# Performance work log

Hardware: AMD Instinct MI355X
Metric: run time of the kernel (lower is better)

## Reference

```python
import jax, jax.numpy as jnp
import numpy as np

B, C, H, W = 2, 192, 64, 64
HEADS, KS = 6, 7
HD = C // HEADS


def setup_inputs() -> dict:
    key = jax.random.key(0)
    ks = jax.random.split(key, 6)
    s = 0.02
    return {
        "x": jax.random.normal(ks[0], (B, C, H, W), jnp.float32),
        "W_qkv1": jax.random.normal(ks[1], (3 * C, C, 1, 1), jnp.float32) * s,
        "b_qkv1": jnp.zeros((3 * C,), jnp.float32),
        "W_qkv2": jax.random.normal(ks[2], (3 * C, 1, 3, 3), jnp.float32) * s,  # depthwise
        "b_qkv2": jnp.zeros((3 * C,), jnp.float32),
        "temperature": jnp.ones((HEADS, 1, 1, 1), jnp.float32),
        "rpb": jax.random.normal(ks[3], (HEADS, 2 * KS - 1, 2 * KS - 1), jnp.float32) * s,
        "W_proj": jax.random.normal(ks[4], (C, C, 1, 1), jnp.float32) * s,
        "b_proj": jnp.zeros((C,), jnp.float32),
    }


def _conv(x, w, b, pad, groups=1):
    y = jax.lax.conv_general_dilated(
        x, w, (1, 1), pad,
        dimension_numbers=("NCHW", "OIHW", "NCHW"),
        feature_group_count=groups)
    return y + b[None, :, None, None]


def _l2norm(t, eps=1e-12):
    n = jnp.sqrt(jnp.sum(t * t, axis=-1, keepdims=True))
    return t / jnp.maximum(n, eps)


def _nbr_idx(L, K):
    # NATTEN shifted-window neighborhood (dilation=1): window start clamped to image.
    start = jnp.clip(jnp.arange(L) - K // 2, 0, L - K)
    idx = start[:, None] + jnp.arange(K)[None, :]        # [L,K] absolute neighbor index
    rel = idx - jnp.arange(L)[:, None] + (K - 1)         # [L,K] rpb table index
    return idx, rel


def _forward(x, W_qkv1, b_qkv1, W_qkv2, b_qkv2, temperature, rpb, W_proj, b_proj):
    Bq, Cq, Hh, Ww = x.shape
    heads = rpb.shape[0]
    K = (rpb.shape[1] + 1) // 2
    hd = Cq // heads
    qkv = _conv(_conv(x, W_qkv1, b_qkv1, "VALID"), W_qkv2, b_qkv2, "SAME", groups=3 * Cq)
    qkv = qkv.reshape(Bq, 3, heads, hd, Hh, Ww).transpose(1, 0, 2, 4, 5, 3)  # [3,B,h,H,W,d]
    q, k, v = qkv[0], qkv[1], qkv[2]
    q = _l2norm(q)
    k = _l2norm(k)
    idx_i, rel_i = _nbr_idx(Hh, K)
    idx_j, rel_j = _nbr_idx(Ww, K)
    ii = idx_i[:, None, :, None]  # [H,1,K,1]
    jj = idx_j[None, :, None, :]  # [1,W,1,K] -> broadcast [H,W,K,K]
    k_nb = k[:, :, ii, jj, :]     # [B,h,H,W,K,K,d]
    attn = jnp.einsum("bhijd,bhijkld->bhijkl", q, k_nb)
    bias = rpb[:, rel_i[:, None, :, None], rel_j[None, :, None, :]]  # [h,H,W,K,K]
    attn = (attn + bias[None]) * temperature.reshape(1, heads, 1, 1, 1, 1)
    attn = jax.nn.softmax(attn.reshape(Bq, heads, Hh, Ww, K * K), axis=-1)
    v_nb = v[:, :, ii, jj, :].reshape(Bq, heads, Hh, Ww, K * K, hd)
    out = jnp.einsum("bhijk,bhijkd->bhijd", attn, v_nb)
    out = out.transpose(0, 1, 4, 2, 3).reshape(Bq, Cq, Hh, Ww)
    return _conv(out, W_proj, b_proj, "VALID")


def reference(x, W_qkv1, b_qkv1, W_qkv2, b_qkv2, temperature, rpb, W_proj, b_proj):
    return _forward(x, W_qkv1, b_qkv1, W_qkv2, b_qkv2, temperature, rpb, W_proj, b_proj)
```

## Files before the change

### kernel.cpp

```cpp
#include <hip/hip_runtime.h>
#include <math.h>

#define HW 4096

typedef __attribute__((ext_vector_type(8))) short short8;
typedef __attribute__((ext_vector_type(8))) _Float16 half8;
typedef __attribute__((ext_vector_type(4))) float floatx4;

__device__ inline float bflo(unsigned u) { return __uint_as_float(u << 16); }
__device__ inline float bfhi(unsigned u) { return __uint_as_float(u & 0xffff0000u); }
__device__ inline unsigned short f2bf(float x) {
    unsigned u = __float_as_uint(x);
    return (unsigned short)((u + 0x7fffu + ((u >> 16) & 1u)) >> 16);
}
__device__ inline unsigned f2bf2(float lo, float hi) {
    unsigned a = __float_as_uint(lo), b = __float_as_uint(hi);
    a = (a + 0x7fffu + ((a >> 16) & 1u)) >> 16;
    b = (b + 0x7fffu + ((b >> 16) & 1u)) & 0xffff0000u;
    return a | b;
}
__device__ inline unsigned short f2h(float x) {
    _Float16 h = (_Float16)x;
    return __builtin_bit_cast(unsigned short, h);
}


__global__ __launch_bounds__(256) void k_gq(const float* __restrict__ x,
    const float* __restrict__ W1, const float* __restrict__ b1,
    unsigned short* __restrict__ qkv)
{
    __shared__ __align__(16) unsigned short As[64 * 200];
    __shared__ __align__(16) unsigned short Bs[64 * 200];
    const int t = threadIdx.x;
    const int m0 = blockIdx.x * 64;
    const int n0 = blockIdx.y * 64;
    const int w = t >> 6, lane = t & 63;
    const int b = m0 >> 12, px0 = m0 & 4095;
    {
        const float* xb = x + ((size_t)(b * 192) << 12) + px0 + lane;
        const int cb = w * 48;
        #pragma unroll
        for (int r4 = 0; r4 < 12; ++r4) {
            float v0 = xb[(size_t)(cb + r4 * 4 + 0) << 12];
            float v1 = xb[(size_t)(cb + r4 * 4 + 1) << 12];
            float v2 = xb[(size_t)(cb + r4 * 4 + 2) << 12];
            float v3 = xb[(size_t)(cb + r4 * 4 + 3) << 12];
            *(uint2*)&As[lane * 200 + cb + r4 * 4] =
                make_uint2(f2bf2(v0, v1), f2bf2(v2, v3));
        }
    }
    #pragma unroll
    for (int pass = 0; pass < 12; ++pass) {
        int idx = pass * 256 + t;
        int row = idx / 48, ch = idx - row * 48;
        float4 wv = *(const float4*)&W1[(size_t)(n0 + row) * 192 + ch * 4];
        *(uint2*)&Bs[row * 200 + ch * 4] =
            make_uint2(f2bf2(wv.x, wv.y), f2bf2(wv.z, wv.w));
    }
    __syncthreads();
    const int lm = lane & 15, lq = lane >> 4;
    floatx4 acc[4] = {};
    #pragma unroll
    for (int ks = 0; ks < 6; ++ks) {
        short8 bf = *(const short8*)&Bs[(w * 16 + lm) * 200 + ks * 32 + lq * 8];
        #pragma unroll
        for (int mt = 0; mt < 4; ++mt) {
            short8 af = *(const short8*)&As[(mt * 16 + lm) * 200 + ks * 32 + lq * 8];
            acc[mt] = __builtin_amdgcn_mfma_f32_16x16x32_bf16(af, bf, acc[mt], 0, 0, 0);
        }
    }
    __syncthreads();
    const float bias = b1[n0 + w * 16 + lm];
    #pragma unroll
    for (int mt = 0; mt < 4; ++mt)
        #pragma unroll
        for (int r = 0; r < 4; ++r)
            As[(mt * 16 + lq * 4 + r) * 72 + w * 16 + lm] = f2bf(acc[mt][r] + bias);
    __syncthreads();
    #pragma unroll
    for (int pass = 0; pass < 2; ++pass) {
        int idx = pass * 256 + t;
        int m = idx >> 3, n8 = idx & 7;
        uint4 val = *(const uint4*)&As[m * 72 + n8 * 8];
        int oc = n0 + n8 * 8;
        int g = oc >> 5, d = oc & 31;
        *(uint4*)&qkv[((((size_t)(b * 18 + g) << 12) + px0 + m) << 5) + d] = val;
    }
}

__global__ __launch_bounds__(256) void k_dw(const unsigned short* __restrict__ in,
    const float* __restrict__ W2, const float* __restrict__ b2,
    unsigned short* __restrict__ outq)
{
    __shared__ float wsm[288];
    __shared__ float bsm[32];
    const int t = threadIdx.x;
    const int bg = blockIdx.y;
    const int g = (bg >= 18) ? bg - 18 : bg;
    const int cbase = (g / 6) * 192 + (g % 6) * 32;
    for (int idx = t; idx < 288; idx += 256)
        wsm[idx] = W2[(cbase + (idx & 31)) * 9 + (idx >> 5)];
    if (t < 32) bsm[t] = b2[cbase + t];
    __syncthreads();
    const int px = (blockIdx.x << 6) + (t >> 2);
    const int d8 = t & 3;
    const int i = px >> 6, j = px & 63;
    const unsigned short* base = in + ((size_t)bg << 17);
    float acc[8];
    #pragma unroll
    for (int e = 0; e < 8; ++e) acc[e] = bsm[d8 * 8 + e];
    #pragma unroll
    for (int di = -1; di <= 1; ++di) {
        int ii = i + di;
        if (ii < 0 || ii > 63) continue;
        #pragma unroll
        for (int dj = -1; dj <= 1; ++dj) {
            int jj = j + dj;
            if (jj < 0 || jj > 63) continue;
            int tap = (di + 1) * 3 + dj + 1;
            uint4 u = *(const uint4*)(base + ((((ii << 6) + jj) << 5) + d8 * 8));
            const float* wt = &wsm[tap * 32 + d8 * 8];
            acc[0] = fmaf(bflo(u.x), wt[0], acc[0]);
            acc[1] = fmaf(bfhi(u.x), wt[1], acc[1]);
            acc[2] = fmaf(bflo(u.y), wt[2], acc[2]);
            acc[3] = fmaf(bfhi(u.y), wt[3], acc[3]);
            acc[4] = fmaf(bflo(u.z), wt[4], acc[4]);
            acc[5] = fmaf(bfhi(u.z), wt[5], acc[5]);
            acc[6] = fmaf(bflo(u.w), wt[6], acc[6]);
            acc[7] = fmaf(bfhi(u.w), wt[7], acc[7]);
        }
    }
    uint4 o;
    o.x = f2bf2(acc[0], acc[1]); o.y = f2bf2(acc[2], acc[3]);
    o.z = f2bf2(acc[4], acc[5]); o.w = f2bf2(acc[6], acc[7]);
    *(uint4*)(outq + ((size_t)bg << 17) + ((size_t)px << 5) + d8 * 8) = o;
}

__global__ __launch_bounds__(256) void k_attn(const unsigned short* __restrict__ qkv,
    const float* __restrict__ temp, const float* __restrict__ rpb,
    unsigned short* __restrict__ attnO)
{
    __shared__ __align__(16) char lds[45224];
    unsigned short* Ks  = (unsigned short*)lds;
    unsigned short* Ps  = (unsigned short*)lds;
    unsigned short* Vts = (unsigned short*)(lds + 29696);
    float* rpbs = (float*)(lds + 44544);

    const int t = threadIdx.x;
    const int ti = blockIdx.x >> 3, tj = blockIdx.x & 7;
    const int head = blockIdx.y, b = blockIdx.z;
    const int i0 = ti * 8, j0 = tj * 8;
    const int r0 = min(max(i0 - 3, 0), 50), c0 = min(max(j0 - 3, 0), 50);
    const unsigned short* qpl = qkv + ((size_t)(b * 18 + head) << 17);
    const unsigned short* kpl = qkv + ((size_t)(b * 18 + 6 + head) << 17);
    const unsigned short* vpl = qkv + ((size_t)(b * 18 + 12 + head) << 17);

    if (t < 196) {
        int r = (t * 2341) >> 15, cc = t - r * 14;
        int pix = ((r0 + r) << 6) + (c0 + cc);
        const uint4* kg = (const uint4*)(kpl + (pix << 5));
        const uint4* vg = (const uint4*)(vpl + (pix << 5));
        float kf[32];
        float ss = 0.f;
        #pragma unroll
        for (int q = 0; q < 4; ++q) {
            uint4 ku = kg[q];
            unsigned uu[4] = {ku.x, ku.y, ku.z, ku.w};
            #pragma unroll
            for (int e = 0; e < 4; ++e) {
                float lo = bflo(uu[e]), hi = bfhi(uu[e]);
                kf[q * 8 + e * 2] = lo; kf[q * 8 + e * 2 + 1] = hi;
                ss = fmaf(lo, lo, fmaf(hi, hi, ss));
            }
        }
        float rinv = 1.0f / fmaxf(sqrtf(ss), 1e-12f);
        #pragma unroll
        for (int q = 0; q < 4; ++q) {
            uint4 p;
            p.x = f2bf2(kf[q * 8 + 0] * rinv, kf[q * 8 + 1] * rinv);
            p.y = f2bf2(kf[q * 8 + 2] * rinv, kf[q * 8 + 3] * rinv);
            p.z = f2bf2(kf[q * 8 + 4] * rinv, kf[q * 8 + 5] * rinv);
            p.w = f2bf2(kf[q * 8 + 6] * rinv, kf[q * 8 + 7] * rinv);
            *(uint4*)&Ks[t * 40 + q * 8] = p;
        }
        #pragma unroll
        for (int q = 0; q < 4; ++q) {
            uint4 vu = vg[q];
            unsigned uu[4] = {vu.x, vu.y, vu.z, vu.w};
            #pragma unroll
            for (int e = 0; e < 4; ++e) {
                Vts[(q * 8 + e * 2) * 232 + t]     = f2h(bflo(uu[e]));
                Vts[(q * 8 + e * 2 + 1) * 232 + t] = f2h(bfhi(uu[e]));
            }
        }
    }
    for (int idx = t; idx < 448; idx += 256) {
        int row = (idx * 2341) >> 15;
        int c = idx - row * 14;
        ((unsigned*)(Vts + row * 232))[98 + c] = 0u;
    }
    if (t < 169) rpbs[t] = rpb[head * 169 + t];

    const int w = t >> 6, lane = t & 63;
    const int lm = lane & 15, lq = lane >> 4;
    const int px = w * 16 + lm;
    const int i = i0 + (px >> 3), j = j0 + (px & 7);
    uint4 qu = *(const uint4*)(qpl + ((((i << 6) + j) << 5) + lq * 8));
    float qf[8];
    qf[0] = bflo(qu.x); qf[1] = bfhi(qu.x);
    qf[2] = bflo(qu.y); qf[3] = bfhi(qu.y);
    qf[4] = bflo(qu.z); qf[5] = bfhi(qu.z);
    qf[6] = bflo(qu.w); qf[7] = bfhi(qu.w);
    float qs = 0.f;
    #pragma unroll
    for (int e = 0; e < 8; ++e) qs = fmaf(qf[e], qf[e], qs);
    qs += __shfl_xor(qs, 16);
    qs += __shfl_xor(qs, 32);
    float qinv = 1.0f / fmaxf(sqrtf(qs), 1e-12f);
    short8 bq;
    #pragma unroll
    for (int e = 0; e < 8; ++e) bq[e] = (short)f2bf(qf[e] * qinv);
    __syncthreads();

    floatx4 acc[13];
    #pragma unroll
    for (int mt = 0; mt < 13; ++mt) {
        short8 ak = *(const short8*)&Ks[(mt * 16 + lm) * 40 + lq * 8];
        floatx4 z = {0.f, 0.f, 0.f, 0.f};
        acc[mt] = __builtin_amdgcn_mfma_f32_16x16x32_bf16(ak, bq, z, 0, 0, 0);
    }
    __syncthreads();

    const int si = min(max(i - 3, 0), 57), sj = min(max(j - 3, 0), 57);
    const int vloi = si - r0, vloj = sj - c0;
    const int oi = r0 - i + 6, oj = c0 - j + 6;
    const float th = temp[head];
    float mx = -1e30f;
    #pragma unroll
    for (int mt = 0; mt < 13; ++mt) {
        int nb0 = mt * 16 + lq * 4;
        int rh0 = (nb0 * 2341) >> 15;
        int ch0 = nb0 - rh0 * 14;
        #pragma unroll
        for (int r = 0; r < 4; ++r) {
            int ch = ch0 + r, rh = rh0;
            if (ch >= 14) { ch -= 14; rh += 1; }
            int bidx = (rh + oi) * 13 + (ch + oj);
            float bias = rpbs[max(0, min(168, bidx))];
            bool valid = ((unsigned)(rh - vloi) <= 6u) && ((unsigned)(ch - vloj) <= 6u);
            float s = (acc[mt][r] + bias) * th;
            s = valid ? s : -1e30f;
            acc[mt][r] = s;
            mx = fmaxf(mx, s);
        }
    }
    mx = fmaxf(mx, __shfl_xor(mx, 16));
    mx = fmaxf(mx, __shfl_xor(mx, 32));
    float ssum = 0.f;
    #pragma unroll
    for (int mt = 0; mt < 13; ++mt)
        #pragma unroll
        for (int r = 0; r < 4; ++r) {
            float e = __expf(acc[mt][r] - mx);
            acc[mt][r] = e;
            ssum += e;
        }
    ssum += __shfl_xor(ssum, 16);
    ssum += __shfl_xor(ssum, 32);
    const float rs = 1.0f / ssum;

    if (lane < 32) {
        uint4 z4 = {0u, 0u, 0u, 0u};
        *(uint4*)&Ps[(w * 16 + (lane >> 1)) * 232 + 208 + (lane & 1) * 8] = z4;
    }
    #pragma unroll
    for (int mt = 0; mt < 13; ++mt) {
        unsigned lo = (unsigned)f2h(acc[mt][0] * rs) | ((unsigned)f2h(acc[mt][1] * rs) << 16);
        unsigned hi = (unsigned)f2h(acc[mt][2] * rs) | ((unsigned)f2h(acc[mt][3] * rs) << 16);
        *(uint2*)&Ps[px * 232 + mt * 16 + lq * 4] = make_uint2(lo, hi);
    }
    __syncthreads();

    floatx4 oacc[2] = {};
    #pragma unroll
    for (int ks = 0; ks < 7; ++ks) {
        half8 ap = *(const half8*)&Ps[(w * 16 + lm) * 232 + ks * 32 + lq * 8];
        #pragma unroll
        for (int n2 = 0; n2 < 2; ++n2) {
            half8 bv = *(const half8*)&Vts[(n2 * 16 + lm) * 232 + ks * 32 + lq * 8];
            oacc[n2] = __builtin_amdgcn_mfma_f32_16x16x32_f16(ap, bv, oacc[n2], 0, 0, 0);
        }
    }
    #pragma unroll
    for (int n2 = 0; n2 < 2; ++n2)
        #pragma unroll
        for (int r = 0; r < 4; ++r) {
            int p2 = w * 16 + lq * 4 + r;
            int i2 = i0 + (p2 >> 3), j2 = j0 + (p2 & 7);
            attnO[((size_t)((b << 12) + (i2 << 6) + j2)) * 192 + head * 32 + n2 * 16 + lm]
                = f2bf(oacc[n2][r]);
        }
}

__global__ __launch_bounds__(256) void k_gp(const unsigned short* __restrict__ Ain,
    const float* __restrict__ Wp, const float* __restrict__ bp,
    float* __restrict__ out)
{
    __shared__ __align__(16) unsigned short As[64 * 200];
    __shared__ __align__(16) unsigned short Bs[64 * 200];
    const int t = threadIdx.x;
    const int m0 = blockIdx.x * 64;
    const int n0 = blockIdx.y * 64;
    #pragma unroll
    for (int pass = 0; pass < 6; ++pass) {
        int idx = pass * 256 + t;
        int m = idx / 24, c16 = idx % 24;
        *(uint4*)&As[m * 200 + c16 * 8] = *(const uint4*)&Ain[(size_t)(m0 + m) * 192 + c16 * 8];
    }
    #pragma unroll
    for (int pass = 0; pass < 12; ++pass) {
        int idx = pass * 256 + t;
        int row = idx / 48, ch = idx - row * 48;
        float4 wv = *(const float4*)&Wp[(size_t)(n0 + row) * 192 + ch * 4];
        *(uint2*)&Bs[row * 200 + ch * 4] =
            make_uint2(f2bf2(wv.x, wv.y), f2bf2(wv.z, wv.w));
    }
    __syncthreads();
    const int w = t >> 6, lane = t & 63;
    const int lm = lane & 15, lq = lane >> 4;
    floatx4 acc[4] = {};
    #pragma unroll
    for (int ks = 0; ks < 6; ++ks) {
        short8 bf = *(const short8*)&Bs[(w * 16 + lm) * 200 + ks * 32 + lq * 8];
        #pragma unroll
        for (int mt = 0; mt < 4; ++mt) {
            short8 af = *(const short8*)&As[(mt * 16 + lm) * 200 + ks * 32 + lq * 8];
            acc[mt] = __builtin_amdgcn_mfma_f32_16x16x32_bf16(af, bf, acc[mt], 0, 0, 0);
        }
    }
    __syncthreads();
    float* fs = (float*)As;
    const float bias = bp[n0 + w * 16 + lm];
    #pragma unroll
    for (int mt = 0; mt < 4; ++mt)
        #pragma unroll
        for (int r = 0; r < 4; ++r)
            fs[(w * 16 + lm) * 68 + mt * 16 + lq * 4 + r] = acc[mt][r] + bias;
    __syncthreads();
    const int b = m0 >> 12, px0 = m0 & 4095;
    #pragma unroll
    for (int pass = 0; pass < 4; ++pass) {
        int idx = pass * 256 + t;
        int n = idx >> 4, m4 = idx & 15;
        float4 val = *(const float4*)&fs[n * 68 + m4 * 4];
        *(float4*)&out[((size_t)(b * 192 + n0 + n) << 12) + px0 + m4 * 4] = val;
    }
}

extern "C" void kernel_launch(void* const* d_in, const int* in_sizes, int n_in,
                              void* d_out, int out_size, void* d_ws, size_t ws_size,
                              hipStream_t stream) {
    const float* x    = (const float*)d_in[0];
    const float* W1   = (const float*)d_in[1];
    const float* b1   = (const float*)d_in[2];
    const float* W2   = (const float*)d_in[3];
    const float* b2   = (const float*)d_in[4];
    const float* temp = (const float*)d_in[5];
    const float* rpb  = (const float*)d_in[6];
    const float* Wp   = (const float*)d_in[7];
    const float* bp   = (const float*)d_in[8];
    float* out = (float*)d_out;

    char* ws = (char*)d_ws;
    unsigned short* qkv1b = (unsigned short*)(ws);
    unsigned short* qkv2b = (unsigned short*)(ws + 9437184);
    unsigned short* attnO = (unsigned short*)(ws + 18874368);

    k_gq  <<<dim3(128, 9), 256, 0, stream>>>(x, W1, b1, qkv1b);
    k_dw  <<<dim3(64, 36), 256, 0, stream>>>(qkv1b, W2, b2, qkv2b);
    k_attn<<<dim3(64, 6, 2), 256, 0, stream>>>(qkv2b, temp, rpb, attnO);
    k_gp  <<<dim3(128, 3), 256, 0, stream>>>(attnO, Wp, bp, out);
}
```

Before: 113.2 us.

## Feed softmax probabilities from registers directly into PV MFMA, dropping LDS staging

The attention kernel used to write normalized probabilities to LDS as a P matrix, synchronise, and reload them for the 16x16x32 f16 PV matrix multiply. It now takes the per-lane accumulator layout of the QK 16x16x32 MFMA output and passes it directly as the A operand of a 16x16x16 f16 MFMA, one per neighbour tile. This removes two block barriers, the LDS round trip for P and the P zero-padding, and shrinks the LDS allocation, which may allow more resident blocks. The cost is more, smaller MFMAs (13×2 instead of 7×2) and narrower V reads, and correctness depends on the accumulator/operand layouts lining up.

```diff
diff --git a/kernel.cpp b/kernel.cpp
--- a/kernel.cpp
+++ b/kernel.cpp
@@ -4,7 +4,7 @@
 #define HW 4096
 
 typedef __attribute__((ext_vector_type(8))) short short8;
-typedef __attribute__((ext_vector_type(8))) _Float16 half8;
+typedef __attribute__((ext_vector_type(4))) _Float16 half4;
 typedef __attribute__((ext_vector_type(4))) float floatx4;
 
 __device__ inline float bflo(unsigned u) { return __uint_as_float(u << 16); }
@@ -140,11 +140,10 @@
     const float* __restrict__ temp, const float* __restrict__ rpb,
     unsigned short* __restrict__ attnO)
 {
-    __shared__ __align__(16) char lds[45224];
+    __shared__ __align__(16) char lds[32164];
     unsigned short* Ks  = (unsigned short*)lds;
-    unsigned short* Ps  = (unsigned short*)lds;
-    unsigned short* Vts = (unsigned short*)(lds + 29696);
-    float* rpbs = (float*)(lds + 44544);
+    unsigned short* Vts = (unsigned short*)(lds + 16640);
+    float* rpbs = (float*)(lds + 31488);
 
     const int t = threadIdx.x;
     const int ti = blockIdx.x >> 3, tj = blockIdx.x & 7;
@@ -194,9 +193,8 @@
             }
         }
     }
-    for (int idx = t; idx < 448; idx += 256) {
-        int row = (idx * 2341) >> 15;
-        int c = idx - row * 14;
+    if (t < 192) {
+        int row = t / 6, c = t - row * 6;
         ((unsigned*)(Vts + row * 232))[98 + c] = 0u;
     }
     if (t < 169) rpbs[t] = rpb[head * 169 + t];
@@ -229,7 +227,6 @@
         floatx4 z = {0.f, 0.f, 0.f, 0.f};
         acc[mt] = __builtin_amdgcn_mfma_f32_16x16x32_bf16(ak, bq, z, 0, 0, 0);
     }
-    __syncthreads();
 
     const int si = min(max(i - 3, 0), 57), sj = min(max(j - 3, 0), 57);
     const int vloi = si - r0, vloj = sj - c0;
@@ -269,26 +266,18 @@
     ssum += __shfl_xor(ssum, 32);
     const float rs = 1.0f / ssum;
 
-    if (lane < 32) {
-        uint4 z4 = {0u, 0u, 0u, 0u};
-        *(uint4*)&Ps[(w * 16 + (lane >> 1)) * 232 + 208 + (lane & 1) * 8] = z4;
-    }
+    floatx4 oacc[2] = {};
     #pragma unroll
     for (int mt = 0; mt < 13; ++mt) {
-        unsigned lo = (unsigned)f2h(acc[mt][0] * rs) | ((unsigned)f2h(acc[mt][1] * rs) << 16);
-        unsigned hi = (unsigned)f2h(acc[mt][2] * rs) | ((unsigned)f2h(acc[mt][3] * rs) << 16);
-        *(uint2*)&Ps[px * 232 + mt * 16 + lq * 4] = make_uint2(lo, hi);
-    }
-    __syncthreads();
-
-    floatx4 oacc[2] = {};
-    #pragma unroll
-    for (int ks = 0; ks < 7; ++ks) {
-        half8 ap = *(const half8*)&Ps[(w * 16 + lm) * 232 + ks * 32 + lq * 8];
+        half4 ap;
+        ap[0] = (_Float16)(acc[mt][0] * rs);
+        ap[1] = (_Float16)(acc[mt][1] * rs);
+        ap[2] = (_Float16)(acc[mt][2] * rs);
+        ap[3] = (_Float16)(acc[mt][3] * rs);
         #pragma unroll
         for (int n2 = 0; n2 < 2; ++n2) {
-            half8 bv = *(const half8*)&Vts[(n2 * 16 + lm) * 232 + ks * 32 + lq * 8];
-            oacc[n2] = __builtin_amdgcn_mfma_f32_16x16x32_f16(ap, bv, oacc[n2], 0, 0, 0);
+            half4 bv = *(const half4*)&Vts[(n2 * 16 + lm) * 232 + mt * 16 + lq * 4];
+            oacc[n2] = __builtin_amdgcn_mfma_f32_16x16x16f16(ap, bv, oacc[n2], 0, 0, 0);
         }
     }
     #pragma unroll
```

Result: no change. 113.3 us (+0.1%).
